# Optimization experiments

Hardware: AMD Instinct MI355X
Metric: run time of the kernel (lower is better)

The kernel has to match this reference:

```python
import jax, jax.numpy as jnp
import numpy as np

N_NODE = 4095
D_EMB = 32
D_MODEL = 64
NHEADS = 8
ALPHA = 1.0
B = N_NODE + 1  # batch must equal n_node+1 (see einsum 'nm,tmd->tnd')
T = 32


def setup_inputs() -> dict:
    key = jax.random.key(0)
    ks = jax.random.split(key, 16)
    f32 = jnp.float32
    inp = {
        "q": jax.random.normal(ks[0], (B, T, D_MODEL), f32),
        "k": jax.random.normal(ks[1], (B, T, D_MODEL), f32),
        "v": jax.random.normal(ks[2], (B, T, D_MODEL), f32),
        # learned parameters (torch init is randn; scaled for numeric stability)
        "emb": jax.random.normal(ks[3], (N_NODE + 1, D_EMB), f32) * 0.05,
        "We": jax.random.normal(ks[4], (D_EMB, D_MODEL, D_MODEL), f32) * 0.05,
        "be": jax.random.normal(ks[5], (D_EMB, D_MODEL), f32) * 0.05,
        "Wq": jax.random.normal(ks[6], (D_MODEL, D_MODEL), f32) * 0.05,
        "bq": jax.random.normal(ks[7], (D_MODEL,), f32) * 0.05,
        "Wk": jax.random.normal(ks[8], (D_MODEL, D_MODEL), f32) * 0.05,
        "bk": jax.random.normal(ks[9], (D_MODEL,), f32) * 0.05,
        "Wv": jax.random.normal(ks[10], (D_MODEL, D_MODEL), f32) * 0.05,
        "bv": jax.random.normal(ks[11], (D_MODEL,), f32) * 0.05,
        "Wo": jax.random.normal(ks[12], (D_MODEL, D_MODEL), f32) * 0.05,
        "bo": jax.random.normal(ks[13], (D_MODEL,), f32) * 0.05,
    }
    return inp


def _elu(x, alpha):
    return jnp.where(x > 0, x, alpha * (jnp.exp(x) - 1.0))


def _split_heads(x, h):
    # torch.cat(torch.split(x, D//h, dim=-1), dim=0): [B,T,D] -> [h*B,T,D/h]
    b, t, d = x.shape
    return jnp.moveaxis(x.reshape(b, t, h, d // h), 2, 0).reshape(h * b, t, d // h)


def _merge_heads(x, b, h):
    # torch.cat(torch.split(x, B, dim=0), dim=-1): [h*B,T,D/h] -> [B,T,D]
    hb, t, dh = x.shape
    return jnp.moveaxis(x.reshape(h, b, t, dh), 0, 2).reshape(b, t, h * dh)


def reference(q, k, v, emb, We, be, Wq, bq, Wk, bk, Wv, bv, Wo, bo):
    Bq, Tq, D = q.shape
    h = NHEADS
    scale = (D // h) ** 0.5

    # linear projections (torch Linear: x @ W.T + b)
    q = q @ Wq.T + bq
    k = k @ Wk.T + bk
    v = v @ Wv.T + bv

    # adjacency: sum over d_emb of pairwise diff == s_i - s_j (same math, no [N,N,E] tensor)
    s = jnp.sum(emb, axis=-1)  # [N+1]
    sim = s[:, None] - s[None, :]  # [N+1, N+1]
    A = jax.nn.softmax(_elu(sim, ALPHA), axis=-1) + jnp.eye(Bq, dtype=q.dtype)

    # updateQ: adjacency-weighted diffusion + per-node weight matrices
    qt = jnp.transpose(q, (1, 0, 2))  # [T, N, D]
    W = jnp.einsum('ne,eio->nio', emb, We)  # [N, D, D]
    b = emb @ be  # [N, D]
    q_ = jnp.einsum('nm,tmd->tnd', A, qt)  # diffusion
    q_ = jnp.einsum('tnd,ndo->tno', q_, W) + b  # per-node matmul
    q = jnp.transpose(q_, (1, 0, 2))  # [N, T, D]

    # manual multi-head attention via split/cat
    qh = _split_heads(q, h)
    kh = _split_heads(k, h)
    vh = _split_heads(v, h)
    attn = jax.nn.softmax(jnp.einsum('btd,bsd->bts', qh, kh) / scale, axis=-1)
    out = jnp.einsum('bts,bsd->btd', attn, vh)
    out = _merge_heads(out, Bq, h)
    return out @ Wo.T + bo
```

## Files before the change

### kernel.cpp

```cpp
#include <hip/hip_runtime.h>
#include <hip/hip_bf16.h>

constexpr int NN  = 4096;
constexpr int DE  = 32;
constexpr int TD  = 2048;

typedef __attribute__((ext_vector_type(8))) short short8;
typedef __attribute__((ext_vector_type(4))) float f32x4;

#define MFMA16(a, b, c) __builtin_amdgcn_mfma_f32_16x16x32_bf16(a, b, c, 0, 0, 0)

__device__ inline ushort f2b(float x) {
    __hip_bfloat16 h = __float2bfloat16(x);
    union { __hip_bfloat16 h; ushort u; } c; c.h = h;
    return c.u;
}

__device__ inline float b2f(ushort u) {
    union { unsigned u; float f; } c; c.u = ((unsigned)u) << 16;
    return c.f;
}

__device__ inline short8 pack8(float4 a, float4 b) {
    short8 v;
    v[0] = (short)f2b(a.x); v[1] = (short)f2b(a.y); v[2] = (short)f2b(a.z); v[3] = (short)f2b(a.w);
    v[4] = (short)f2b(b.x); v[5] = (short)f2b(b.y); v[6] = (short)f2b(b.z); v[7] = (short)f2b(b.w);
    return v;
}

__device__ inline short8 pack8v(f32x4 a, f32x4 b) {
    short8 v;
    v[0] = (short)f2b(a[0]); v[1] = (short)f2b(a[1]); v[2] = (short)f2b(a[2]); v[3] = (short)f2b(a[3]);
    v[4] = (short)f2b(b[0]); v[5] = (short)f2b(b[1]); v[6] = (short)f2b(b[2]); v[7] = (short)f2b(b[3]);
    return v;
}

__device__ __forceinline__ short8 as_s8(f32x4 v) {
    union { f32x4 f; short8 s; } u; u.f = v; return u.s;
}

template<int OFF>
__device__ __forceinline__ f32x4 gl16(unsigned long long addr) {
    f32x4 d;
    asm volatile("global_load_dwordx4 %0, %1, off offset:%c2"
                 : "=v"(d) : "v"(addr), "n"(OFF) : "memory");
    return d;
}

template<int OFF>
__device__ __forceinline__ float gl4(unsigned long long addr) {
    float d;
    asm volatile("global_load_dword %0, %1, off offset:%c2"
                 : "=v"(d) : "v"(addr), "n"(OFF) : "memory");
    return d;
}

#define WAITV(N) asm volatile("s_waitcnt vmcnt(" #N ")" ::: "memory"); \
                 __builtin_amdgcn_sched_barrier(0)

__global__ __launch_bounds__(256) void k_prep(const float* __restrict__ emb,
                                              const float* __restrict__ We,
                                              const float* __restrict__ be,
                                              const float* __restrict__ Wk,
                                              const float* __restrict__ Wv,
                                              const float* __restrict__ Wo,
                                              float* __restrict__ s_g,
                                              ushort* __restrict__ embbf,
                                              ushort* __restrict__ WeTT,
                                              ushort* __restrict__ Wkbf,
                                              ushort* __restrict__ Wvbf,
                                              ushort* __restrict__ Wobf,
                                              float* __restrict__ bn) {
    int id = blockIdx.x, tid = threadIdx.x;
    if (id < 16) {
        int n = id * 256 + tid;
        const float4* e4 = (const float4*)(emb + n * DE);
        float s = 0.f;
#pragma unroll
        for (int i = 0; i < DE / 4; ++i) { float4 v = e4[i]; s += v.x + v.y + v.z + v.w; }
        s_g[n] = s;
    } else if (id < 144) {
        int g4 = (id - 16) * 256 + tid;
        float4 v = *(const float4*)&emb[(size_t)g4 * 4];
        ushort4 o; o.x = f2b(v.x); o.y = f2b(v.y); o.z = f2b(v.z); o.w = f2b(v.w);
        *(ushort4*)&embbf[(size_t)g4 * 4] = o;
    } else if (id < 176) {
        int e = id - 144;
#pragma unroll
        for (int u = 0; u < 4; ++u) {
            int idx0 = tid * 16 + u * 4;
            float4 v = *(const float4*)&We[(size_t)e * 4096 + idx0];
            float vv[4] = {v.x, v.y, v.z, v.w};
#pragma unroll
            for (int i = 0; i < 4; ++i) {
                int idx = idx0 + i;
                int o = idx & 63, d = idx >> 6;
                WeTT[(size_t)(o * 64 + d) * 32 + e] = f2b(vv[i]);
            }
        }
    } else if (id < 224) {
        int id5 = id - 176;
        int which = id5 >> 4, gid = (id5 & 15) * 256 + tid;
        const float* src = which == 0 ? Wk : (which == 1 ? Wv : Wo);
        ushort* dst = which == 0 ? Wkbf : (which == 1 ? Wvbf : Wobf);
        dst[gid] = f2b(src[gid]);
    } else {
        int gid = (id - 224) * 256 + tid;
        int n = gid >> 6, o = gid & 63;
        float acc = 0.f;
#pragma unroll
        for (int e = 0; e < DE; ++e) acc += emb[n * DE + e] * be[e * 64 + o];
        bn[gid] = acc;
    }
}

__global__ __launch_bounds__(256) void k_pr(const float* __restrict__ X,
                                            const float* __restrict__ W,
                                            const float* __restrict__ bias,
                                            ushort* __restrict__ Y,
                                            const float* __restrict__ s_g,
                                            int* __restrict__ perm) {
    __shared__ float ss[NN];
    int id = blockIdx.x, tid = threadIdx.x;
    if (id < 512) {
        int lane = tid & 63, wid = tid >> 6;
        int r0 = id * 256 + wid * 64;
        int l15 = lane & 15, kb = lane >> 4;
        f32x4 acc[4][4] = {};
#pragma unroll
        for (int kk = 0; kk < 2; ++kk) {
            short8 af[4], bf[4];
#pragma unroll
            for (int f = 0; f < 4; ++f) {
                const float* ap = X + (size_t)(r0 + f * 16 + l15) * 64 + kk * 32 + kb * 8;
                af[f] = pack8(*(const float4*)ap, *(const float4*)(ap + 4));
                const float* bp = W + (size_t)(f * 16 + l15) * 64 + kk * 32 + kb * 8;
                bf[f] = pack8(*(const float4*)bp, *(const float4*)(bp + 4));
            }
#pragma unroll
            for (int i = 0; i < 4; ++i)
#pragma unroll
                for (int j = 0; j < 4; ++j)
                    acc[i][j] = MFMA16(af[i], bf[j], acc[i][j]);
        }
        float bcol[4];
#pragma unroll
        for (int j = 0; j < 4; ++j) bcol[j] = bias[j * 16 + l15];
#pragma unroll
        for (int i = 0; i < 4; ++i)
#pragma unroll
            for (int j = 0; j < 4; ++j)
#pragma unroll
                for (int r = 0; r < 4; ++r)
                    Y[(size_t)(r0 + i * 16 + kb * 4 + r) * 64 + j * 16 + l15] =
                        f2b(acc[i][j][r] + bcol[j]);
    } else {
        for (int i = tid; i < NN; i += 256) ss[i] = s_g[i];
        __syncthreads();
        int g = tid >> 5, l = tid & 31;
        int n = (id - 512) * 8 + g;
        float sn = ss[n];
        int cnt = 0;
        for (int j2 = 0; j2 < 128; ++j2) {
            int m = j2 * 32 + l;
            float sm = ss[m];
            cnt += (sm < sn) || (sm == sn && m < n);
        }
        for (int off = 16; off; off >>= 1) cnt += __shfl_down(cnt, off, 32);
        if (l == 0) perm[cnt] = n;
    }
}

__global__ __launch_bounds__(256) void k_csum(const ushort* __restrict__ qp,
                                              const float* __restrict__ s_g,
                                              const int* __restrict__ perm,
                                              float* __restrict__ Cj,
                                              float* __restrict__ Cb) {
    __shared__ int ns[32];
    __shared__ float bs[32];
    int bx = blockIdx.x, by = blockIdx.y, tid = threadIdx.x;
    if (tid < 32) {
        int n = perm[bx * 32 + tid];
        ns[tid] = n;
        bs[tid] = __expf(-s_g[n]);
    }
    __syncthreads();
    int j = by * 256 + tid;
    float run[8] = {};
    for (int ii = 0; ii < 32; ++ii) {
        float qv = b2f(qp[(size_t)ns[ii] * 2048 + j]);
        float b = bs[ii], t = qv;
#pragma unroll
        for (int k2 = 0; k2 < 8; ++k2) { run[k2] += t; t *= b; }
    }
    float* cp = Cj + ((size_t)bx * 2048 + j) * 8;
    *(float4*)cp       = make_float4(run[0], run[1], run[2], run[3]);
    *(float4*)(cp + 4) = make_float4(run[4], run[5], run[6], run[7]);
    if (by == 0 && tid < 32) {
        float b = bs[tid], bk = 1.f;
#pragma unroll
        for (int k2 = 0; k2 < 8; ++k2) {
            float v = bk;
            for (int off = 16; off; off >>= 1) v += __shfl_down(v, off, 32);
            if (tid == 0) Cb[bx * 8 + k2] = v;
            bk *= b;
        }
    }
}

__global__ __launch_bounds__(256) void k_pre(const float* __restrict__ Cj,
                                             float* __restrict__ PRE,
                                             const float* __restrict__ Cb,
                                             float* __restrict__ CbPre) {
    __shared__ float sCb[1024];
    int tid = threadIdx.x;
    if (blockIdx.x < 64) {
        int gid = blockIdx.x * 256 + tid;
        float run = 0.f;
#pragma unroll 8
        for (int c = 0; c < 128; ++c) {
            PRE[(size_t)c * 16384 + gid] = run;
            run += Cj[(size_t)c * 16384 + gid];
        }
        PRE[(size_t)128 * 16384 + gid] = run;
    } else {
        sCb[tid] = Cb[tid];
        sCb[tid + 256] = Cb[tid + 256];
        sCb[tid + 512] = Cb[tid + 512];
        sCb[tid + 768] = Cb[tid + 768];
        __syncthreads();
        if (tid < 8) {
            float run = 0.f;
            for (int c = 0; c < 128; ++c) {
                CbPre[c * 8 + tid] = run;
                run += sCb[c * 8 + tid];
            }
            CbPre[1024 + tid] = run;
        }
    }
}

__global__ __launch_bounds__(256) void k_combw(const ushort* __restrict__ qp,
                                               const float* __restrict__ s_g,
                                               const int* __restrict__ perm,
                                               const float* __restrict__ PRE,
                                               const float* __restrict__ CbPre,
                                               ushort* __restrict__ qdifb,
                                               const ushort* __restrict__ embbf,
                                               const ushort* __restrict__ WeTT,
                                               ushort* __restrict__ WnT) {
    __shared__ int ns[32];
    __shared__ float sa[32], sb[32];
    int id = blockIdx.x, tid = threadIdx.x;
    if (id < 1024) {
        int bx = id & 127, by = id >> 7;
        if (tid < 32) {
            int n = perm[bx * 32 + tid];
            ns[tid] = n;
            float s = s_g[n];
            sa[tid] = __expf(s);
            sb[tid] = __expf(-s);
        }
        __syncthreads();
        int j = by * 256 + tid;
        float T[8], pre[8];
        {
            const float* pp = PRE + (size_t)bx * 16384 + (size_t)j * 8;
            float4 u0 = *(const float4*)pp, u1 = *(const float4*)(pp + 4);
            pre[0] = u0.x; pre[1] = u0.y; pre[2] = u0.z; pre[3] = u0.w;
            pre[4] = u1.x; pre[5] = u1.y; pre[6] = u1.z; pre[7] = u1.w;
            const float* tp = PRE + (size_t)128 * 16384 + (size_t)j * 8;
            float4 t0 = *(const float4*)tp, t1 = *(const float4*)(tp + 4);
            T[0] = t0.x; T[1] = t0.y; T[2] = t0.z; T[3] = t0.w;
            T[4] = t1.x; T[5] = t1.y; T[6] = t1.z; T[7] = t1.w;
        }
        float TB[8], preb[8];
        {
            float4 v0 = *(const float4*)&CbPre[bx * 8], v1 = *(const float4*)&CbPre[bx * 8 + 4];
            preb[0] = v0.x; preb[1] = v0.y; preb[2] = v0.z; preb[3] = v0.w;
            preb[4] = v1.x; preb[5] = v1.y; preb[6] = v1.z; preb[7] = v1.w;
            float4 t0 = *(const float4*)&CbPre[1024], t1 = *(const float4*)&CbPre[1028];
            TB[0] = t0.x; TB[1] = t0.y; TB[2] = t0.z; TB[3] = t0.w;
            TB[4] = t1.x; TB[5] = t1.y; TB[6] = t1.z; TB[7] = t1.w;
        }
#pragma unroll 2
        for (int ii = 0; ii < 32; ++ii) {
            int n = ns[ii];
            float a = sa[ii], b = sb[ii];
            float g0 = 0.36787944117144233f;
            float g1 = g0 * a;
            float g2 = g1 * a * 0.5f;
            float g3 = g2 * a * (1.f / 3.f);
            float g4 = g3 * a * 0.25f;
            float g5 = g4 * a * 0.2f;
            float g6 = g5 * a * (1.f / 6.f);
            float g7 = g6 * a * (1.f / 7.f);
            float Z = a * preb[1]
                    + g0 * (TB[0] - preb[0]) + g1 * (TB[1] - preb[1])
                    + g2 * (TB[2] - preb[2]) + g3 * (TB[3] - preb[3])
                    + g4 * (TB[4] - preb[4]) + g5 * (TB[5] - preb[5])
                    + g6 * (TB[6] - preb[6]) + g7 * (TB[7] - preb[7]);
            float izv = 1.f / Z;
            float qv = b2f(qp[(size_t)n * 2048 + j]);
            float ss2 = g0 * (T[0] - pre[0]) + g1 * (T[1] - pre[1])
                      + g2 * (T[2] - pre[2]) + g3 * (T[3] - pre[3])
                      + g4 * (T[4] - pre[4]) + g5 * (T[5] - pre[5])
                      + g6 * (T[6] - pre[6]) + g7 * (T[7] - pre[7]);
            float outv = (a * pre[1] + ss2) * izv + qv;
            qdifb[(size_t)n * 2048 + j] = f2b(outv);
            float bk = 1.f;
#pragma unroll
            for (int k2 = 0; k2 < 8; ++k2) { pre[k2] += bk * qv; preb[k2] += bk; bk *= b; }
        }
    } else {
        int w2 = id - 1024;
        int lane = tid & 63, wid = tid >> 6;
        int n0  = (w2 & 31) * 128 + (wid >> 1) * 64;
        int od0 = (w2 >> 5) * 128 + (wid & 1) * 64;
        int l15 = lane & 15, kb = lane >> 4;
        short8 af[4], bf[4];
#pragma unroll
        for (int f = 0; f < 4; ++f) {
            af[f] = *(const short8*)(embbf + (size_t)(n0 + f * 16 + l15) * 32 + kb * 8);
            bf[f] = *(const short8*)(WeTT + (size_t)(od0 + f * 16 + l15) * 32 + kb * 8);
        }
        f32x4 acc[4][4] = {};
#pragma unroll
        for (int i = 0; i < 4; ++i)
#pragma unroll
            for (int j = 0; j < 4; ++j)
                acc[i][j] = MFMA16(af[i], bf[j], acc[i][j]);
#pragma unroll
        for (int i = 0; i < 4; ++i)
#pragma unroll
            for (int j = 0; j < 4; ++j)
#pragma unroll
                for (int r = 0; r < 4; ++r)
                    WnT[(size_t)(n0 + i * 16 + kb * 4 + r) * 4096 + od0 + j * 16 + l15] =
                        f2b(acc[i][j][r]);
    }
}

__global__ __launch_bounds__(256, 2) void k_fused(const float* __restrict__ kin,
                                                  const float* __restrict__ vin,
                                                  const ushort* __restrict__ qdifb,
                                                  const ushort* __restrict__ WnT,
                                                  const float* __restrict__ bn,
                                                  const ushort* __restrict__ Wkbf,
                                                  const float* __restrict__ bk,
                                                  const ushort* __restrict__ Wvbf,
                                                  const float* __restrict__ bv,
                                                  const ushort* __restrict__ Wobf,
                                                  const float* __restrict__ bo,
                                                  float* __restrict__ out) {
    __shared__ ushort Kb[2176];
    __shared__ ushort Qb[2176];
    __shared__ ushort Vb[2560];
    __shared__ ushort Pb[4][1280];
    __shared__ ushort attb[2304];
    int tid = threadIdx.x, lane = tid & 63, w = tid >> 6;
    int b = blockIdx.x;
    int l15 = lane & 15, g = lane >> 4;
    int hh_w = l15 >> 3, d1_w = l15 & 7;
    const float SCALE = 0.35355339059327373f;
    short8 zfrag = {};

    f32x4 wx0, wx1, wx2, wx3, wx4, wx5, wx6, wx7;
    f32x4 x0, x1, x2, x3, x4, x5, x6, x7;
    float bxc0, bxc1, bxc2, bxc3;
    f32x4 q0v, q1v, q2v, q3v;
    f32x4 wn0, wn1, wn2, wn3;
    float bnc0, bnc1;
    f32x4 wo0, wo1; float boc;

    if (w < 2) {
        const float*  xin = w ? vin : kin;
        const ushort* Wx  = w ? Wvbf : Wkbf;
        const float*  bx_ = w ? bv : bk;
        unsigned long long bxA = (unsigned long long)(bx_ + l15);
        unsigned long long wxA = (unsigned long long)((const char*)Wx + l15 * 128 + g * 16 + 3072);
        unsigned long long xaA = (unsigned long long)(xin + (size_t)b * TD + (8 + l15) * 64 + g * 8);
        bxc0 = gl4<0>(bxA); bxc1 = gl4<64>(bxA); bxc2 = gl4<128>(bxA); bxc3 = gl4<192>(bxA);
        wx0 = gl16<-3072>(wxA); wx1 = gl16<-3008>(wxA);
        wx2 = gl16<-1024>(wxA); wx3 = gl16< -960>(wxA);
        wx4 = gl16< 1024>(wxA); wx5 = gl16< 1088>(wxA);
        wx6 = gl16< 3072>(wxA); wx7 = gl16< 3136>(wxA);
        x0 = gl16<-2048>(xaA); x1 = gl16<-2032>(xaA);
        x2 = gl16<-1920>(xaA); x3 = gl16<-1904>(xaA);
        x4 = gl16< 2048>(xaA); x5 = gl16< 2064>(xaA);
        x6 = gl16< 2176>(xaA); x7 = gl16< 2192>(xaA);
    } else {
        int wq = w - 2;
        unsigned long long qaA = (unsigned long long)(qdifb + (size_t)b * TD + (8 + l15) * 64 + g * 8);
        unsigned long long wnA = (unsigned long long)((const char*)(WnT + (size_t)b * 4096)
                                                      + ((size_t)(wq * 32 + l15)) * 128 + g * 16);
        unsigned long long bnA = (unsigned long long)(bn + (size_t)b * 64 + wq * 32 + l15);
        q0v = gl16<-1024>(qaA); q1v = gl16<-960>(qaA);
        q2v = gl16< 1024>(qaA); q3v = gl16<1088>(qaA);
        wn0 = gl16<0>(wnA); wn1 = gl16<64>(wnA);
        wn2 = gl16<2048>(wnA); wn3 = gl16<2112>(wnA);
        bnc0 = gl4<0>(bnA); bnc1 = gl4<64>(bnA);
    }
    {
        unsigned long long woA = (unsigned long long)((const char*)Wobf
                                                      + ((size_t)(w * 16 + l15)) * 128 + g * 16);
        unsigned long long boA = (unsigned long long)(bo + w * 16 + l15);
        wo0 = gl16<0>(woA); wo1 = gl16<64>(woA);
        boc = gl4<0>(boA);
    }

    if (w < 2) {
        WAITV(3);
        short8 xaf[2][2], wxf[4][2];
        xaf[0][0] = pack8v(x0, x1); xaf[1][0] = pack8v(x2, x3);
        xaf[0][1] = pack8v(x4, x5); xaf[1][1] = pack8v(x6, x7);
        wxf[0][0] = as_s8(wx0); wxf[0][1] = as_s8(wx1);
        wxf[1][0] = as_s8(wx2); wxf[1][1] = as_s8(wx3);
        wxf[2][0] = as_s8(wx4); wxf[2][1] = as_s8(wx5);
        wxf[3][0] = as_s8(wx6); wxf[3][1] = as_s8(wx7);
        float bxc[4] = {bxc0, bxc1, bxc2, bxc3};
#pragma unroll
        for (int j = 0; j < 4; ++j) {
            f32x4 ax[2] = {};
#pragma unroll
            for (int kk = 0; kk < 2; ++kk)
#pragma unroll
                for (int ti = 0; ti < 2; ++ti)
                    ax[ti] = MFMA16(xaf[kk][ti], wxf[j][kk], ax[ti]);
            if (w == 0) {
#pragma unroll
                for (int ti = 0; ti < 2; ++ti)
#pragma unroll
                    for (int r = 0; r < 4; ++r) {
                        int s = ti * 16 + g * 4 + r;
                        Kb[(j * 2 + hh_w) * 272 + s * 8 + d1_w] = f2b(ax[ti][r] + bxc[j]);
                    }
            } else {
#pragma unroll
                for (int ti = 0; ti < 2; ++ti)
#pragma unroll
                    for (int r = 0; r < 4; r += 2) {
                        int s = ti * 16 + g * 4 + r;
                        ushort2 p; p.x = f2b(ax[ti][r] + bxc[j]); p.y = f2b(ax[ti][r + 1] + bxc[j]);
                        *(ushort2*)&Vb[(j * 2 + hh_w) * 320 + d1_w * 40 + s] = p;
                    }
            }
        }
    } else {
        int wq = w - 2;
        WAITV(3);
        short8 qaf[2][2], wnf[2][2];
        qaf[0][0] = as_s8(q0v); qaf[1][0] = as_s8(q1v);
        qaf[0][1] = as_s8(q2v); qaf[1][1] = as_s8(q3v);
        wnf[0][0] = as_s8(wn0); wnf[0][1] = as_s8(wn1);
        wnf[1][0] = as_s8(wn2); wnf[1][1] = as_s8(wn3);
        float bnc[2] = {bnc0, bnc1};
#pragma unroll
        for (int jj = 0; jj < 2; ++jj) {
            int j = 2 * wq + jj;
            f32x4 aq[2] = {};
#pragma unroll
            for (int kk = 0; kk < 2; ++kk)
#pragma unroll
                for (int ti = 0; ti < 2; ++ti)
                    aq[ti] = MFMA16(qaf[kk][ti], wnf[jj][kk], aq[ti]);
#pragma unroll
            for (int ti = 0; ti < 2; ++ti)
#pragma unroll
                for (int r = 0; r < 4; ++r) {
                    int s = ti * 16 + g * 4 + r;
                    Qb[(j * 2 + hh_w) * 272 + s * 8 + d1_w] = f2b(aq[ti][r] + bnc[jj]);
                }
        }
    }
    __syncthreads();

#pragma unroll
    for (int hh = 0; hh < 2; ++hh) {
        int h = 2 * w + hh;
        short8 kf[2], qf[2];
#pragma unroll
        for (int si = 0; si < 2; ++si)
            kf[si] = (lane < 16) ? *(const short8*)&Kb[h * 272 + (si * 16 + l15) * 8] : zfrag;
#pragma unroll
        for (int ti = 0; ti < 2; ++ti)
            qf[ti] = (lane < 16) ? *(const short8*)&Qb[h * 272 + (ti * 16 + l15) * 8] : zfrag;
        f32x4 sc[2][2];
#pragma unroll
        for (int si = 0; si < 2; ++si)
#pragma unroll
            for (int ti = 0; ti < 2; ++ti)
                sc[si][ti] = MFMA16(kf[si], qf[ti], f32x4{});
#pragma unroll
        for (int ti = 0; ti < 2; ++ti) {
            float e0[4], e1[4], sm = 0.f;
#pragma unroll
            for (int r = 0; r < 4; ++r) {
                e0[r] = __expf(sc[0][ti][r] * SCALE);
                e1[r] = __expf(sc[1][ti][r] * SCALE);
                sm += e0[r] + e1[r];
            }
            sm += __shfl_xor(sm, 16);
            sm += __shfl_xor(sm, 32);
            float inv = 1.f / sm;
            int t = ti * 16 + l15;
            unsigned p00 = (unsigned)f2b(e0[0] * inv) | ((unsigned)f2b(e0[1] * inv) << 16);
            unsigned p01 = (unsigned)f2b(e0[2] * inv) | ((unsigned)f2b(e0[3] * inv) << 16);
            unsigned p10 = (unsigned)f2b(e1[0] * inv) | ((unsigned)f2b(e1[1] * inv) << 16);
            unsigned p11 = (unsigned)f2b(e1[2] * inv) | ((unsigned)f2b(e1[3] * inv) << 16);
            *(unsigned*)&Pb[w][t * 40 + g * 4]          = p00;
            *(unsigned*)&Pb[w][t * 40 + g * 4 + 2]      = p01;
            *(unsigned*)&Pb[w][t * 40 + 16 + g * 4]     = p10;
            *(unsigned*)&Pb[w][t * 40 + 16 + g * 4 + 2] = p11;
        }
        short8 vf = *(const short8*)&Vb[h * 320 + (l15 & 7) * 40 + g * 8];
#pragma unroll
        for (int ti = 0; ti < 2; ++ti) {
            short8 af = *(const short8*)&Pb[w][(ti * 16 + l15) * 40 + g * 8];
            f32x4 pv = MFMA16(af, vf, f32x4{});
            if (l15 < 8) {
#pragma unroll
                for (int r = 0; r < 4; ++r)
                    attb[(ti * 16 + g * 4 + r) * 72 + h * 8 + l15] = f2b(pv[r]);
            }
        }
    }
    __syncthreads();

    WAITV(0);
    {
        short8 wof[2];
        wof[0] = as_s8(wo0); wof[1] = as_s8(wo1);
        short8 aof[2][2];
#pragma unroll
        for (int kk = 0; kk < 2; ++kk)
#pragma unroll
            for (int ti = 0; ti < 2; ++ti)
                aof[kk][ti] = *(const short8*)&attb[(ti * 16 + l15) * 72 + kk * 32 + g * 8];
        f32x4 co[2] = {};
#pragma unroll
        for (int kk = 0; kk < 2; ++kk)
#pragma unroll
            for (int ti = 0; ti < 2; ++ti)
                co[ti] = MFMA16(aof[kk][ti], wof[kk], co[ti]);
#pragma unroll
        for (int ti = 0; ti < 2; ++ti)
#pragma unroll
            for (int r = 0; r < 4; ++r)
                out[(size_t)b * TD + (ti * 16 + g * 4 + r) * 64 + w * 16 + l15] =
                    co[ti][r] + boc;
    }
}

extern "C" void kernel_launch(void* const* d_in, const int* in_sizes, int n_in,
                              void* d_out, int out_size, void* d_ws, size_t ws_size,
                              hipStream_t stream) {
    const float* q   = (const float*)d_in[0];
    const float* k   = (const float*)d_in[1];
    const float* v   = (const float*)d_in[2];
    const float* emb = (const float*)d_in[3];
    const float* We  = (const float*)d_in[4];
    const float* be  = (const float*)d_in[5];
    const float* Wq  = (const float*)d_in[6];
    const float* bq  = (const float*)d_in[7];
    const float* Wk  = (const float*)d_in[8];
    const float* bk  = (const float*)d_in[9];
    const float* Wv  = (const float*)d_in[10];
    const float* bv  = (const float*)d_in[11];
    const float* Wo  = (const float*)d_in[12];
    const float* bo  = (const float*)d_in[13];

    float* ws = (float*)d_ws;
    ushort* qp    = (ushort*)ws;
    ushort* WnT   = (ushort*)(ws + 4194304);
    ushort* qdifb = (ushort*)(ws + 12582912);
    float*  Cj    = ws + 16777216;
    float*  bn    = ws + 18874368;
    float*  s_g   = ws + 19136512;
    int*    perm  = (int*)(ws + 19140608);
    float*  Cb    = ws + 19144704;
    ushort* embbf = (ushort*)(ws + 19145728);
    ushort* WeTT  = (ushort*)(ws + 19211264);
    ushort* Wkbf  = (ushort*)(ws + 19276800);
    ushort* Wvbf  = (ushort*)(ws + 19278848);
    ushort* Wobf  = (ushort*)(ws + 19280896);
    float*  PRE   = ws + 19282944;
    float*  CbPre = ws + 21396480;
    float*  outp  = (float*)d_out;

    k_prep <<<1248, 256, 0, stream>>>(emb, We, be, Wk, Wv, Wo,
                                      s_g, embbf, WeTT, Wkbf, Wvbf, Wobf, bn);
    k_pr   <<<1024, 256, 0, stream>>>(q, Wq, bq, qp, s_g, perm);
    k_csum <<<dim3(128, 8), 256, 0, stream>>>(qp, s_g, perm, Cj, Cb);
    k_pre  <<<65, 256, 0, stream>>>(Cj, PRE, Cb, CbPre);
    k_combw<<<2048, 256, 0, stream>>>(qp, s_g, perm, PRE, CbPre, qdifb,
                                      embbf, WeTT, WnT);
    k_fused<<<4096, 256, 0, stream>>>(k, v, qdifb, WnT, bn,
                                      Wkbf, bk, Wvbf, bv, Wobf, bo, outp);
}
```

Before: 104.6 us.

## Merge prep and projection kernels, recompute sums locally, move bn to MFMA

Merges k_prep and k_pr into one launch. The rank-sort blocks now recompute the per-node embedding sums into shared memory themselves, so they no longer depend on s_g written by another block. Each thread now counts the rank for one node over the whole array, replacing the old 32-lane reduction with shuffles. The emb@be bias is moved from a scalar loop into extra MFMA blocks inside k_combw. This removes one kernel launch and the scalar bias work, at the cost of redundant sum computation (each of 16 blocks reads all of emb) and longer serial rank loops per thread.

```diff
diff --git a/kernel.cpp b/kernel.cpp
--- a/kernel.cpp
+++ b/kernel.cpp
@@ -58,23 +58,27 @@
 #define WAITV(N) asm volatile("s_waitcnt vmcnt(" #N ")" ::: "memory"); \
                  __builtin_amdgcn_sched_barrier(0)
 
-__global__ __launch_bounds__(256) void k_prep(const float* __restrict__ emb,
-                                              const float* __restrict__ We,
-                                              const float* __restrict__ be,
-                                              const float* __restrict__ Wk,
-                                              const float* __restrict__ Wv,
-                                              const float* __restrict__ Wo,
-                                              float* __restrict__ s_g,
-                                              ushort* __restrict__ embbf,
-                                              ushort* __restrict__ WeTT,
-                                              ushort* __restrict__ Wkbf,
-                                              ushort* __restrict__ Wvbf,
-                                              ushort* __restrict__ Wobf,
-                                              float* __restrict__ bn) {
+__global__ __launch_bounds__(256) void k_prep2(const float* __restrict__ q,
+                                               const float* __restrict__ Wq,
+                                               const float* __restrict__ bq,
+                                               const float* __restrict__ emb,
+                                               const float* __restrict__ We,
+                                               const float* __restrict__ Wk,
+                                               const float* __restrict__ Wv,
+                                               const float* __restrict__ Wo,
+                                               float* __restrict__ s_g,
+                                               ushort* __restrict__ embbf,
+                                               ushort* __restrict__ WeTT,
+                                               ushort* __restrict__ Wkbf,
+                                               ushort* __restrict__ Wvbf,
+                                               ushort* __restrict__ Wobf,
+                                               ushort* __restrict__ qp,
+                                               int* __restrict__ perm) {
+    __shared__ float ss[NN];
     int id = blockIdx.x, tid = threadIdx.x;
     if (id < 16) {
         int n = id * 256 + tid;
-        const float4* e4 = (const float4*)(emb + n * DE);
+        const float4* e4 = (const float4*)(emb + (size_t)n * DE);
         float s = 0.f;
 #pragma unroll
         for (int i = 0; i < DE / 4; ++i) { float4 v = e4[i]; s += v.x + v.y + v.z + v.w; }
@@ -104,27 +108,9 @@
         const float* src = which == 0 ? Wk : (which == 1 ? Wv : Wo);
         ushort* dst = which == 0 ? Wkbf : (which == 1 ? Wvbf : Wobf);
         dst[gid] = f2b(src[gid]);
-    } else {
-        int gid = (id - 224) * 256 + tid;
-        int n = gid >> 6, o = gid & 63;
-        float acc = 0.f;
-#pragma unroll
-        for (int e = 0; e < DE; ++e) acc += emb[n * DE + e] * be[e * 64 + o];
-        bn[gid] = acc;
-    }
-}
-
-__global__ __launch_bounds__(256) void k_pr(const float* __restrict__ X,
-                                            const float* __restrict__ W,
-                                            const float* __restrict__ bias,
-                                            ushort* __restrict__ Y,
-                                            const float* __restrict__ s_g,
-                                            int* __restrict__ perm) {
-    __shared__ float ss[NN];
-    int id = blockIdx.x, tid = threadIdx.x;
-    if (id < 512) {
+    } else if (id < 736) {
         int lane = tid & 63, wid = tid >> 6;
-        int r0 = id * 256 + wid * 64;
+        int r0 = (id - 224) * 256 + wid * 64;
         int l15 = lane & 15, kb = lane >> 4;
         f32x4 acc[4][4] = {};
 #pragma unroll
@@ -132,9 +118,9 @@
             short8 af[4], bf[4];
 #pragma unroll
             for (int f = 0; f < 4; ++f) {
-                const float* ap = X + (size_t)(r0 + f * 16 + l15) * 64 + kk * 32 + kb * 8;
+                const float* ap = q + (size_t)(r0 + f * 16 + l15) * 64 + kk * 32 + kb * 8;
                 af[f] = pack8(*(const float4*)ap, *(const float4*)(ap + 4));
-                const float* bp = W + (size_t)(f * 16 + l15) * 64 + kk * 32 + kb * 8;
+                const float* bp = Wq + (size_t)(f * 16 + l15) * 64 + kk * 32 + kb * 8;
                 bf[f] = pack8(*(const float4*)bp, *(const float4*)(bp + 4));
             }
 #pragma unroll
@@ -145,29 +131,35 @@
         }
         float bcol[4];
 #pragma unroll
-        for (int j = 0; j < 4; ++j) bcol[j] = bias[j * 16 + l15];
+        for (int j = 0; j < 4; ++j) bcol[j] = bq[j * 16 + l15];
 #pragma unroll
         for (int i = 0; i < 4; ++i)
 #pragma unroll
             for (int j = 0; j < 4; ++j)
 #pragma unroll
                 for (int r = 0; r < 4; ++r)
-                    Y[(size_t)(r0 + i * 16 + kb * 4 + r) * 64 + j * 16 + l15] =
+                    qp[(size_t)(r0 + i * 16 + kb * 4 + r) * 64 + j * 16 + l15] =
                         f2b(acc[i][j][r] + bcol[j]);
     } else {
-        for (int i = tid; i < NN; i += 256) ss[i] = s_g[i];
+        for (int row = tid; row < NN; row += 256) {
+            const float4* e4 = (const float4*)(emb + (size_t)row * DE);
+            float s = 0.f;
+#pragma unroll
+            for (int i = 0; i < DE / 4; ++i) { float4 v = e4[i]; s += v.x + v.y + v.z + v.w; }
+            ss[row] = s;
+        }
         __syncthreads();
-        int g = tid >> 5, l = tid & 31;
-        int n = (id - 512) * 8 + g;
+        int n = (id - 736) * 256 + tid;
         float sn = ss[n];
         int cnt = 0;
-        for (int j2 = 0; j2 < 128; ++j2) {
-            int m = j2 * 32 + l;
-            float sm = ss[m];
-            cnt += (sm < sn) || (sm == sn && m < n);
-        }
-        for (int off = 16; off; off >>= 1) cnt += __shfl_down(cnt, off, 32);
-        if (l == 0) perm[cnt] = n;
+        for (int m4 = 0; m4 < NN; m4 += 4) {
+            float4 sm = *(const float4*)&ss[m4];
+            cnt += (sm.x < sn) || (sm.x == sn && (m4 + 0) < n);
+            cnt += (sm.y < sn) || (sm.y == sn && (m4 + 1) < n);
+            cnt += (sm.z < sn) || (sm.z == sn && (m4 + 2) < n);
+            cnt += (sm.w < sn) || (sm.w == sn && (m4 + 3) < n);
+        }
+        perm[cnt] = n;
     }
 }
 
@@ -248,7 +240,9 @@
                                                ushort* __restrict__ qdifb,
                                                const ushort* __restrict__ embbf,
                                                const ushort* __restrict__ WeTT,
-                                               ushort* __restrict__ WnT) {
+                                               ushort* __restrict__ WnT,
+                                               const float* __restrict__ be,
+                                               float* __restrict__ bn) {
     __shared__ int ns[32];
     __shared__ float sa[32], sb[32];
     int id = blockIdx.x, tid = threadIdx.x;
@@ -312,7 +306,7 @@
 #pragma unroll
             for (int k2 = 0; k2 < 8; ++k2) { pre[k2] += bk * qv; preb[k2] += bk; bk *= b; }
         }
-    } else {
+    } else if (id < 2048) {
         int w2 = id - 1024;
         int lane = tid & 63, wid = tid >> 6;
         int n0  = (w2 & 31) * 128 + (wid >> 1) * 64;
@@ -338,6 +332,36 @@
                 for (int r = 0; r < 4; ++r)
                     WnT[(size_t)(n0 + i * 16 + kb * 4 + r) * 4096 + od0 + j * 16 + l15] =
                         f2b(acc[i][j][r]);
+    } else {
+        int blk = id - 2048;
+        int lane = tid & 63, wid = tid >> 6;
+        int n0 = blk * 256 + wid * 64;
+        int l15 = lane & 15, kb = lane >> 4;
+        short8 af[4], bf[4];
+#pragma unroll
+        for (int f = 0; f < 4; ++f)
+            af[f] = *(const short8*)(embbf + (size_t)(n0 + f * 16 + l15) * 32 + kb * 8);
+#pragma unroll
+        for (int j = 0; j < 4; ++j) {
+            short8 v;
+#pragma unroll
+            for (int i = 0; i < 8; ++i)
+                v[i] = (short)f2b(be[(kb * 8 + i) * 64 + j * 16 + l15]);
+            bf[j] = v;
+        }
+        f32x4 acc[4][4] = {};
+#pragma unroll
+        for (int i = 0; i < 4; ++i)
+#pragma unroll
+            for (int j = 0; j < 4; ++j)
+                acc[i][j] = MFMA16(af[i], bf[j], acc[i][j]);
+#pragma unroll
+        for (int i = 0; i < 4; ++i)
+#pragma unroll
+            for (int j = 0; j < 4; ++j)
+#pragma unroll
+                for (int r = 0; r < 4; ++r)
+                    bn[(size_t)(n0 + i * 16 + kb * 4 + r) * 64 + j * 16 + l15] = acc[i][j][r];
     }
 }
 
@@ -588,13 +612,12 @@
     float*  CbPre = ws + 21396480;
     float*  outp  = (float*)d_out;
 
-    k_prep <<<1248, 256, 0, stream>>>(emb, We, be, Wk, Wv, Wo,
-                                      s_g, embbf, WeTT, Wkbf, Wvbf, Wobf, bn);
-    k_pr   <<<1024, 256, 0, stream>>>(q, Wq, bq, qp, s_g, perm);
+    k_prep2<<<752, 256, 0, stream>>>(q, Wq, bq, emb, We, Wk, Wv, Wo,
+                                     s_g, embbf, WeTT, Wkbf, Wvbf, Wobf, qp, perm);
     k_csum <<<dim3(128, 8), 256, 0, stream>>>(qp, s_g, perm, Cj, Cb);
     k_pre  <<<65, 256, 0, stream>>>(Cj, PRE, Cb, CbPre);
-    k_combw<<<2048, 256, 0, stream>>>(qp, s_g, perm, PRE, CbPre, qdifb,
-                                      embbf, WeTT, WnT);
+    k_combw<<<2064, 256, 0, stream>>>(qp, s_g, perm, PRE, CbPre, qdifb,
+                                      embbf, WeTT, WnT, be, bn);
     k_fused<<<4096, 256, 0, stream>>>(k, v, qdifb, WnT, bn,
                                       Wkbf, bk, Wvbf, bv, Wobf, bo, outp);
 }
```

Result: slower. 203.0 us (+94.1%).
